# Performance work log

Hardware: AMD Instinct MI355X
Metric: run time of the kernel (lower is better)

The kernel has to match this reference:

```python
import jax, jax.numpy as jnp
import numpy as np

# Module dims (match init_kwargs): c_in=1, khop=3, f=128, c_out=2, f_out=128
N, KHOP, NNB, C_IN, F_IN = 2048, 3, 16, 1, 128
C_OUT, F_OUT = 2, 128
EPS_ROOT, EPS_NORM = 1e-8, 1e-7


def setup_inputs() -> dict:
    key = jax.random.key(0)
    k1, k2, k3 = jax.random.split(key, 3)
    x = jax.random.normal(k1, (N, C_IN, F_IN), jnp.float32)
    # dense form of the ragged neighbor[i][k] -> (n, c, f) lists
    neighbor = jax.random.normal(k2, (N, KHOP, NNB, C_IN, F_IN), jnp.float32)
    # Conv1d(khop*c_in, c_out*f_out, kernel_size=f, bias=False) weight
    W = jax.random.normal(k3, (C_OUT * F_OUT, KHOP * C_IN, F_IN), jnp.float32) * 0.05
    return {"x": x, "neighbor": neighbor, "W": W}


def _sgnroot(a):
    return jnp.sign(a) * jnp.sqrt(jnp.clip(jnp.abs(a), EPS_ROOT))


def _row_normalize(a):
    a = a / (jnp.abs(a).sum(-2, keepdims=True) + EPS_NORM)
    return jnp.where(jnp.isnan(a), 0.0, a)


def _feature_adjacency(x, neighbor):
    # x: (N,c,f), neighbor: (N,k,n,c,f) -> fadj: (N,k,f,f)
    fadj = jnp.einsum('Nca,Nkncb->Nkab', x, neighbor)
    fadj = fadj + jnp.swapaxes(fadj, -1, -2)
    return _row_normalize(_sgnroot(fadj))


def _transform(z, adj, W):
    # z: (..., c, f); adj: (..., K, f, f) broadcastable against z's batch dims
    # y[..., K, c, a] = sum_b adj[..., K, a, b] * z[..., c, b]
    y = jnp.einsum('...kab,...cb->...kca', adj, z)
    y = y.reshape(y.shape[:-3] + (KHOP * C_IN, F_IN))  # (..., k*c, f)
    # Conv1d with kernel_size == f and output length 1 == full contraction
    out = jnp.einsum('oqf,...qf->...o', W, y)
    return out.reshape(out.shape[:-1] + (C_OUT, F_OUT))


def reference(x, neighbor, W):
    adj = _feature_adjacency(x, neighbor)                     # (N,k,f,f)
    x_out = _transform(x, adj, W)                             # (N,c_out,f_out)
    # each neighbor[i,k] is transformed with the full per-sample adj[i]
    nbr_out = _transform(neighbor, adj[:, None, None], W)     # (N,k,n,c_out,f_out)
    return (x_out, nbr_out)
```

## Files before the change

### kernel.cpp

```cpp
#include <hip/hip_runtime.h>

typedef unsigned short u16;
typedef unsigned int u32;
typedef __bf16 bf16;
typedef __bf16 bf16x8 __attribute__((ext_vector_type(8)));
typedef __bf16 bf16x4 __attribute__((ext_vector_type(4)));
typedef float f32x4 __attribute__((ext_vector_type(4)));

#define NSAMP 2048
#define KH 3
#define NNBR 16
#define F 128
#define OUT_O 256
#define QT 384

#define ZLD 136
#define YLD 136

__device__ __forceinline__ bf16x4 cvt4(float4 v) {
    bf16x4 h;
    h[0] = (bf16)v.x; h[1] = (bf16)v.y; h[2] = (bf16)v.z; h[3] = (bf16)v.w;
    return h;
}

__global__ void wprep(const float* __restrict__ W, bf16* __restrict__ Wbf) {
    int i = blockIdx.x * 256 + threadIdx.x;
    if (i < OUT_O * QT) Wbf[i] = (bf16)W[i];
}

__launch_bounds__(512, 4)
__global__ void featkhop(const float* __restrict__ xg,
                         const float* __restrict__ ng,
                         const bf16* __restrict__ Wbf,
                         float* __restrict__ out) {
    __shared__ __align__(16) bf16 Zs[64 * ZLD];
    __shared__ __align__(16) bf16 Ys[2][64 * YLD];
    float* const xls = (float*)(Zs + 49 * ZLD);
    float* const sls = xls + F;
    float* const rsi = xls + 4 * F;

    const int i = blockIdx.x;
    const int t = threadIdx.x;
    const int lane = t & 63;
    const int w = t >> 6;
    const int lr = lane & 15;
    const int lg = lane >> 4;

    if (t < F / 4) {
        float4 v = *(const float4*)(xg + (size_t)i * F + t * 4);
        *(float4*)(xls + t * 4) = v;
        *(bf16x4*)(Zs + 0 * ZLD + t * 4) = cvt4(v);
    }
    {
        const float* nb = ng + (size_t)i * (KH * NNBR * F);
        #pragma unroll
        for (int c = 0; c < 3; ++c) {
            int j = c * 512 + t;
            float4 v = *(const float4*)(nb + j * 4);
            int fl = j * 4;
            int row = 1 + (fl >> 7);
            int b = fl & 127;
            *(bf16x4*)(Zs + row * ZLD + b) = cvt4(v);
        }
    }
    __syncthreads();

    if (t < KH * F) {
        int q = t >> 7, b = t & 127;
        float s = 0.f;
        #pragma unroll
        for (int n = 0; n < NNBR; ++n) s += (float)Zs[(1 + q * NNBR + n) * ZLD + b];
        sls[q * F + b] = s;
    }
    __syncthreads();

    const int a_row = w * 16 + lr;
    const float x_a = xls[a_row];
    const int cbase = lg * 8;

    #pragma unroll
    for (int q = 0; q < KH; ++q) {
        const float s_a = sls[q * F + a_row];
        float ps = 0.f;
        #pragma unroll
        for (int kk = 0; kk < 4; ++kk) {
            float4 xb0 = *(const float4*)(xls + kk * 32 + cbase);
            float4 xb1 = *(const float4*)(xls + kk * 32 + cbase + 4);
            float4 sb0 = *(const float4*)(sls + q * F + kk * 32 + cbase);
            float4 sb1 = *(const float4*)(sls + q * F + kk * 32 + cbase + 4);
            float xb[8] = {xb0.x, xb0.y, xb0.z, xb0.w, xb1.x, xb1.y, xb1.z, xb1.w};
            float sb[8] = {sb0.x, sb0.y, sb0.z, sb0.w, sb1.x, sb1.y, sb1.z, sb1.w};
            #pragma unroll
            for (int e = 0; e < 8; ++e) {
                float tv = x_a * sb[e] + xb[e] * s_a;
                ps += __builtin_amdgcn_sqrtf(fmaxf(fabsf(tv), 1e-8f));
            }
        }
        ps += __shfl_xor(ps, 16);
        ps += __shfl_xor(ps, 32);
        if (lg == 0) rsi[q * F + a_row] = __builtin_amdgcn_rcpf(ps + 1e-7f);
    }
    __syncthreads();

    f32x4 acc2[4][2];
    {
        f32x4 zf = {0.f, 0.f, 0.f, 0.f};
        #pragma unroll
        for (int mt = 0; mt < 4; ++mt) { acc2[mt][0] = zf; acc2[mt][1] = zf; }
    }

    for (int q = 0; q < KH; ++q) {
        const float s_a = sls[q * F + a_row];
        bf16x8 bfrag[4];
        #pragma unroll
        for (int kk = 0; kk < 4; ++kk) {
            float4 xb0 = *(const float4*)(xls + kk * 32 + cbase);
            float4 xb1 = *(const float4*)(xls + kk * 32 + cbase + 4);
            float4 sb0 = *(const float4*)(sls + q * F + kk * 32 + cbase);
            float4 sb1 = *(const float4*)(sls + q * F + kk * 32 + cbase + 4);
            float4 rb0 = *(const float4*)(rsi + q * F + kk * 32 + cbase);
            float4 rb1 = *(const float4*)(rsi + q * F + kk * 32 + cbase + 4);
            float xb[8] = {xb0.x, xb0.y, xb0.z, xb0.w, xb1.x, xb1.y, xb1.z, xb1.w};
            float sb[8] = {sb0.x, sb0.y, sb0.z, sb0.w, sb1.x, sb1.y, sb1.z, sb1.w};
            float rb[8] = {rb0.x, rb0.y, rb0.z, rb0.w, rb1.x, rb1.y, rb1.z, rb1.w};
            #pragma unroll
            for (int e = 0; e < 8; ++e) {
                float tv = x_a * sb[e] + xb[e] * s_a;
                float r = tv * __builtin_amdgcn_rsqf(fmaxf(fabsf(tv), 1e-8f));
                bfrag[kk][e] = (bf16)(r * rb[e]);
            }
        }

        bf16* Ysb = Ys[q & 1];
        f32x4 acc1[4];
        {
            f32x4 zf = {0.f, 0.f, 0.f, 0.f};
            #pragma unroll
            for (int mt = 0; mt < 4; ++mt) acc1[mt] = zf;
        }
        #pragma unroll
        for (int kk = 0; kk < 4; ++kk) {
            #pragma unroll
            for (int mt = 0; mt < 4; ++mt) {
                bf16x8 af = *(const bf16x8*)(Zs + (mt * 16 + lr) * ZLD + kk * 32 + cbase);
                acc1[mt] = __builtin_amdgcn_mfma_f32_16x16x32_bf16(af, bfrag[kk], acc1[mt], 0, 0, 0);
            }
        }
        #pragma unroll
        for (int mt = 0; mt < 4; ++mt) {
            #pragma unroll
            for (int r = 0; r < 4; ++r)
                Ysb[(mt * 16 + lg * 4 + r) * YLD + w * 16 + lr] = (bf16)acc1[mt][r];
        }
        __syncthreads();

        #pragma unroll
        for (int kk = 0; kk < 4; ++kk) {
            const bf16* wp = Wbf + (size_t)(w * 32 + lr) * QT + q * F + kk * 32 + cbase;
            bf16x8 bf0 = *(const bf16x8*)wp;
            bf16x8 bf1 = *(const bf16x8*)(wp + 16 * QT);
            #pragma unroll
            for (int mt = 0; mt < 4; ++mt) {
                bf16x8 af = *(const bf16x8*)(Ysb + (mt * 16 + lr) * YLD + kk * 32 + cbase);
                acc2[mt][0] = __builtin_amdgcn_mfma_f32_16x16x32_bf16(af, bf0, acc2[mt][0], 0, 0, 0);
                acc2[mt][1] = __builtin_amdgcn_mfma_f32_16x16x32_bf16(af, bf1, acc2[mt][1], 0, 0, 0);
            }
        }
    }

    float* xout = out + (size_t)i * OUT_O;
    float* nout = out + (size_t)NSAMP * OUT_O + (size_t)i * 48 * OUT_O;
    #pragma unroll
    for (int mt = 0; mt < 4; ++mt) {
        #pragma unroll
        for (int r = 0; r < 4; ++r) {
            int v = mt * 16 + lg * 4 + r;
            #pragma unroll
            for (int nn = 0; nn < 2; ++nn) {
                int o = w * 32 + nn * 16 + lr;
                float val = acc2[mt][nn][r];
                if (v == 0) xout[o] = val;
                else if (v <= 48) nout[(size_t)(v - 1) * OUT_O + o] = val;
            }
        }
    }
}

extern "C" void kernel_launch(void* const* d_in, const int* in_sizes, int n_in,
                              void* d_out, int out_size, void* d_ws, size_t ws_size,
                              hipStream_t stream) {
    const float* x   = (const float*)d_in[0];
    const float* nbr = (const float*)d_in[1];
    const float* W   = (const float*)d_in[2];
    bf16* Wbf = (bf16*)d_ws;
    wprep<<<(OUT_O * QT + 255) / 256, 256, 0, stream>>>(W, Wbf);
    featkhop<<<NSAMP, 512, 0, stream>>>(x, nbr, Wbf, (float*)d_out);
}
```

Baseline: 84.25 us.

## Fuse W bf16 conversion into main kernel and vectorize Y stores via operand swap

Removes the separate W-to-bf16 prep kernel and converts fp32 W to bf16 in registers inside the main kernel, with the loads hoisted before the barrier. The first MFMA's operands are swapped so each lane writes four contiguous bf16 values into shared Y. The neighbor column sums read global memory directly, which drops one block barrier, and the q loop is unrolled. In exchange each block reads W in fp32, doubling weight traffic, and register pressure rises.

```diff
diff --git a/kernel.cpp b/kernel.cpp
--- a/kernel.cpp
+++ b/kernel.cpp
@@ -23,15 +23,10 @@
     return h;
 }
 
-__global__ void wprep(const float* __restrict__ W, bf16* __restrict__ Wbf) {
-    int i = blockIdx.x * 256 + threadIdx.x;
-    if (i < OUT_O * QT) Wbf[i] = (bf16)W[i];
-}
-
 __launch_bounds__(512, 4)
 __global__ void featkhop(const float* __restrict__ xg,
                          const float* __restrict__ ng,
-                         const bf16* __restrict__ Wbf,
+                         const float* __restrict__ Wg,
                          float* __restrict__ out) {
     __shared__ __align__(16) bf16 Zs[64 * ZLD];
     __shared__ __align__(16) bf16 Ys[2][64 * YLD];
@@ -51,8 +46,8 @@
         *(float4*)(xls + t * 4) = v;
         *(bf16x4*)(Zs + 0 * ZLD + t * 4) = cvt4(v);
     }
+    const float* nb = ng + (size_t)i * (KH * NNBR * F);
     {
-        const float* nb = ng + (size_t)i * (KH * NNBR * F);
         #pragma unroll
         for (int c = 0; c < 3; ++c) {
             int j = c * 512 + t;
@@ -63,13 +58,11 @@
             *(bf16x4*)(Zs + row * ZLD + b) = cvt4(v);
         }
     }
-    __syncthreads();
-
     if (t < KH * F) {
         int q = t >> 7, b = t & 127;
         float s = 0.f;
         #pragma unroll
-        for (int n = 0; n < NNBR; ++n) s += (float)Zs[(1 + q * NNBR + n) * ZLD + b];
+        for (int n = 0; n < NNBR; ++n) s += nb[(q * NNBR + n) * F + b];
         sls[q * F + b] = s;
     }
     __syncthreads();
@@ -109,9 +102,10 @@
         for (int mt = 0; mt < 4; ++mt) { acc2[mt][0] = zf; acc2[mt][1] = zf; }
     }
 
+    #pragma unroll
     for (int q = 0; q < KH; ++q) {
         const float s_a = sls[q * F + a_row];
-        bf16x8 bfrag[4];
+        bf16x8 afrag[4];
         #pragma unroll
         for (int kk = 0; kk < 4; ++kk) {
             float4 xb0 = *(const float4*)(xls + kk * 32 + cbase);
@@ -127,7 +121,7 @@
             for (int e = 0; e < 8; ++e) {
                 float tv = x_a * sb[e] + xb[e] * s_a;
                 float r = tv * __builtin_amdgcn_rsqf(fmaxf(fabsf(tv), 1e-8f));
-                bfrag[kk][e] = (bf16)(r * rb[e]);
+                afrag[kk][e] = (bf16)(r * rb[e]);
             }
         }
 
@@ -142,28 +136,45 @@
         for (int kk = 0; kk < 4; ++kk) {
             #pragma unroll
             for (int mt = 0; mt < 4; ++mt) {
-                bf16x8 af = *(const bf16x8*)(Zs + (mt * 16 + lr) * ZLD + kk * 32 + cbase);
-                acc1[mt] = __builtin_amdgcn_mfma_f32_16x16x32_bf16(af, bfrag[kk], acc1[mt], 0, 0, 0);
-            }
-        }
+                bf16x8 zfrag = *(const bf16x8*)(Zs + (mt * 16 + lr) * ZLD + kk * 32 + cbase);
+                acc1[mt] = __builtin_amdgcn_mfma_f32_16x16x32_bf16(afrag[kk], zfrag, acc1[mt], 0, 0, 0);
+            }
+        }
+
+        bf16x8 wf0[4], wf1[4];
+        #pragma unroll
+        for (int kk = 0; kk < 4; ++kk) {
+            const float* wp = Wg + (size_t)(w * 32 + lr) * QT + q * F + kk * 32 + cbase;
+            float4 a0 = *(const float4*)(wp);
+            float4 a1 = *(const float4*)(wp + 4);
+            float4 b0 = *(const float4*)(wp + 16 * QT);
+            float4 b1 = *(const float4*)(wp + 16 * QT + 4);
+            wf0[kk][0] = (bf16)a0.x; wf0[kk][1] = (bf16)a0.y;
+            wf0[kk][2] = (bf16)a0.z; wf0[kk][3] = (bf16)a0.w;
+            wf0[kk][4] = (bf16)a1.x; wf0[kk][5] = (bf16)a1.y;
+            wf0[kk][6] = (bf16)a1.z; wf0[kk][7] = (bf16)a1.w;
+            wf1[kk][0] = (bf16)b0.x; wf1[kk][1] = (bf16)b0.y;
+            wf1[kk][2] = (bf16)b0.z; wf1[kk][3] = (bf16)b0.w;
+            wf1[kk][4] = (bf16)b1.x; wf1[kk][5] = (bf16)b1.y;
+            wf1[kk][6] = (bf16)b1.z; wf1[kk][7] = (bf16)b1.w;
+        }
+
         #pragma unroll
         for (int mt = 0; mt < 4; ++mt) {
-            #pragma unroll
-            for (int r = 0; r < 4; ++r)
-                Ysb[(mt * 16 + lg * 4 + r) * YLD + w * 16 + lr] = (bf16)acc1[mt][r];
+            bf16x4 yv;
+            #pragma unroll
+            for (int r = 0; r < 4; ++r) yv[r] = (bf16)acc1[mt][r];
+            *(bf16x4*)(Ysb + (mt * 16 + lr) * YLD + w * 16 + lg * 4) = yv;
         }
         __syncthreads();
 
         #pragma unroll
         for (int kk = 0; kk < 4; ++kk) {
-            const bf16* wp = Wbf + (size_t)(w * 32 + lr) * QT + q * F + kk * 32 + cbase;
-            bf16x8 bf0 = *(const bf16x8*)wp;
-            bf16x8 bf1 = *(const bf16x8*)(wp + 16 * QT);
             #pragma unroll
             for (int mt = 0; mt < 4; ++mt) {
                 bf16x8 af = *(const bf16x8*)(Ysb + (mt * 16 + lr) * YLD + kk * 32 + cbase);
-                acc2[mt][0] = __builtin_amdgcn_mfma_f32_16x16x32_bf16(af, bf0, acc2[mt][0], 0, 0, 0);
-                acc2[mt][1] = __builtin_amdgcn_mfma_f32_16x16x32_bf16(af, bf1, acc2[mt][1], 0, 0, 0);
+                acc2[mt][0] = __builtin_amdgcn_mfma_f32_16x16x32_bf16(af, wf0[kk], acc2[mt][0], 0, 0, 0);
+                acc2[mt][1] = __builtin_amdgcn_mfma_f32_16x16x32_bf16(af, wf1[kk], acc2[mt][1], 0, 0, 0);
             }
         }
     }
@@ -192,7 +203,5 @@
     const float* x   = (const float*)d_in[0];
     const float* nbr = (const float*)d_in[1];
     const float* W   = (const float*)d_in[2];
-    bf16* Wbf = (bf16*)d_ws;
-    wprep<<<(OUT_O * QT + 255) / 256, 256, 0, stream>>>(W, Wbf);
-    featkhop<<<NSAMP, 512, 0, stream>>>(x, nbr, Wbf, (float*)d_out);
+    featkhop<<<NSAMP, 512, 0, stream>>>(x, nbr, W, (float*)d_out);
 }
```

Result: slower. 109.8 us (+30.3%).
